# Kernel tuning notes

Hardware: AMD Instinct MI355X
Metric: run time of the kernel (lower is better)

Reference implementation:

```python
import jax, jax.numpy as jnp
import numpy as np

N_ATOMS = 100000   # real atoms (row 0 is padding => arrays have +1)
N_BONDS = 200000   # directed bonds (row 0 is padding)
MAX_NB = 6         # max incoming bonds per atom
ATOM_FDIM = 133
BOND_FDIM = 147
HIDDEN = 300
DEPTH = 3
NUM_MOLS = 2048


def setup_inputs() -> dict:
    key = jax.random.key(0)
    ks = jax.random.split(key, 10)
    f_atoms = jax.random.normal(ks[0], (N_ATOMS + 1, ATOM_FDIM), jnp.float32)
    f_bonds = jax.random.normal(ks[1], (N_BONDS + 1, BOND_FDIM), jnp.float32)
    # zero padding row, as in chemprop's BatchMolGraph
    f_atoms = f_atoms.at[0].set(0.0)
    f_bonds = f_bonds.at[0].set(0.0)
    W_i = jax.random.normal(ks[2], (BOND_FDIM, HIDDEN), jnp.float32) * 0.05
    W_h = jax.random.normal(ks[3], (HIDDEN, HIDDEN), jnp.float32) * 0.05
    W_o = jax.random.normal(ks[4], (ATOM_FDIM + HIDDEN, HIDDEN), jnp.float32) * 0.05
    b_o = jax.random.normal(ks[5], (HIDDEN,), jnp.float32) * 0.05
    a2b = jax.random.randint(ks[6], (N_ATOMS + 1, MAX_NB), 0, N_BONDS + 1, jnp.int32)
    b2a = jax.random.randint(ks[7], (N_BONDS + 1,), 0, N_ATOMS + 1, jnp.int32)
    b2revb = jax.random.randint(ks[8], (N_BONDS + 1,), 0, N_BONDS + 1, jnp.int32)
    # padding rows point at padding
    a2b = a2b.at[0].set(0)
    b2a = b2a.at[0].set(0)
    b2revb = b2revb.at[0].set(0)
    mol_ids = jax.random.randint(ks[9], (N_ATOMS,), 0, NUM_MOLS, jnp.int32)
    return {"f_atoms": f_atoms, "f_bonds": f_bonds, "W_i": W_i, "W_h": W_h,
            "W_o": W_o, "b_o": b_o, "a2b": a2b, "b2a": b2a,
            "b2revb": b2revb, "mol_ids": mol_ids}


def reference(f_atoms, f_bonds, W_i, W_h, W_o, b_o, a2b, b2a, b2revb, mol_ids):
    act = jax.nn.relu
    # input bond messages (W_i has no bias: args.bias=False)
    b_input = f_bonds @ W_i                      # [B+1, H]
    b_message = act(b_input)
    for _ in range(DEPTH - 1):
        # gather incoming bond messages per atom and sum over neighbors
        nei_a_message = b_message[a2b]           # [A+1, MAX_NB, H]
        a_message = nei_a_message.sum(axis=1)    # [A+1, H]
        # directed message update: m_uv = sum_in(v) - m_vu
        b_message = a_message[b2a] - b_message[b2revb]
        b_message = b_message @ W_h
        b_message = act(b_input + b_message)     # dropout p=0 omitted
    # atom readout
    nei_a_message = b_message[a2b]
    a_message = nei_a_message.sum(axis=1)        # [A+1, H]
    a_input = jnp.concatenate([f_atoms, a_message], axis=1)
    atom_hiddens = act(a_input @ W_o + b_o)      # [A+1, H]
    # mean-pool per molecule (a_scope readout), excluding padding row 0
    h = atom_hiddens[1:]                         # [A, H]
    sums = jax.ops.segment_sum(h, mol_ids, num_segments=NUM_MOLS)
    counts = jax.ops.segment_sum(jnp.ones((h.shape[0],), h.dtype), mol_ids,
                                 num_segments=NUM_MOLS)
    mol_vecs = sums / jnp.maximum(counts, 1.0)[:, None]  # [NUM_MOLS, H]
    return mol_vecs
```

## Files before the change

### kernel.cpp

```cpp
#include <hip/hip_runtime.h>

constexpr int N_ATOMS = 100000;
constexpr int NATOMS1 = 100001;
constexpr int NBONDS1 = 200001;
constexpr int MAXNB   = 6;
constexpr int AF      = 133;
constexpr int BF      = 147;
constexpr int H       = 300;
constexpr int NMOL    = 2048;
constexpr int KP      = 448;
constexpr int NP      = 320;
constexpr int QCOL_B  = 148;
constexpr int QCOL_A  = 136;
constexpr int QH      = 75;

typedef unsigned short u16;
typedef unsigned int   u32;
typedef __attribute__((ext_vector_type(8))) short bh8;
typedef __attribute__((ext_vector_type(4))) float f32x4;

__device__ inline float b2f(u16 h) {
    union { u32 u; float f; } x; x.u = ((u32)h) << 16; return x.f;
}
__device__ inline u16 f2b(float f) {
    union { float f; u32 u; } x; x.f = f;
    return (u16)((x.u + 0x7FFFu + ((x.u >> 16) & 1u)) >> 16);
}

template<bool HAS_BIAS>
__global__ __launch_bounds__(256, 2)
void mfma_gemm_k(const u16* __restrict__ A, const u16* __restrict__ Wt,
                 const float* __restrict__ bias, u16* __restrict__ out, int M)
{
    __shared__ __align__(16) unsigned char smem[48 * 1024];
    const int tid  = threadIdx.x;
    const int lane = tid & 63;
    const int w    = tid >> 6;
    const int row0 = blockIdx.x * 64;

    f32x4 acc[4][5];
    #pragma unroll
    for (int i = 0; i < 4; ++i)
        #pragma unroll
        for (int j = 0; j < 5; ++j)
            acc[i][j] = (f32x4)0.f;

    for (int kt = 0; kt < KP / 64; ++kt) {
        const int k0 = kt * 64;
        #pragma unroll
        for (int i = 0; i < 2; ++i) {
            int cid = tid + 256 * i;
            int r   = cid & 63;
            int kk  = cid >> 6;
            int ks  = kk >> 2, sub = kk & 3;
            uint4 v = {0u, 0u, 0u, 0u};
            int row = row0 + r;
            if (row < M) v = *(const uint4*)(A + (size_t)row * KP + k0 + kk * 8);
            *(uint4*)(smem + (((r >> 4) * 2 + ks) * 1024) + sub * 256 + (r & 15) * 16) = v;
        }
        #pragma unroll
        for (int i = 0; i < 10; ++i) {
            int cid = tid + 256 * i;
            int kk  = cid / 320;
            int col = cid - kk * 320;
            int ks  = kk >> 2, sub = kk & 3;
            uint4 v = *(const uint4*)(Wt + (size_t)col * KP + k0 + kk * 8);
            *(uint4*)(smem + 8192 + (((col >> 4) * 2 + ks) * 1024) + sub * 256 + (col & 15) * 16) = v;
        }
        __syncthreads();
        #pragma unroll
        for (int ks = 0; ks < 2; ++ks) {
            bh8 af[4], bf_[5];
            #pragma unroll
            for (int fm = 0; fm < 4; ++fm)
                af[fm] = *(const bh8*)(smem + (fm * 2 + ks) * 1024 + lane * 16);
            #pragma unroll
            for (int cf = 0; cf < 5; ++cf)
                bf_[cf] = *(const bh8*)(smem + 8192 + ((w * 5 + cf) * 2 + ks) * 1024 + lane * 16);
            #pragma unroll
            for (int fm = 0; fm < 4; ++fm)
                #pragma unroll
                for (int cf = 0; cf < 5; ++cf)
                    acc[fm][cf] = __builtin_amdgcn_mfma_f32_16x16x32_bf16(
                        af[fm], bf_[cf], acc[fm][cf], 0, 0, 0);
        }
        __syncthreads();
    }

    const int r4  = (lane >> 4) * 4;
    const int c15 = lane & 15;
    #pragma unroll
    for (int cf = 0; cf < 5; ++cf) {
        int col = w * 80 + cf * 16 + c15;
        if (col >= H) continue;
        float bv = HAS_BIAS ? bias[col] : 0.f;
        #pragma unroll
        for (int fm = 0; fm < 4; ++fm) {
            #pragma unroll
            for (int i = 0; i < 4; ++i) {
                int row = row0 + fm * 16 + r4 + i;
                if (row < M)
                    out[(size_t)row * H + col] = f2b(fmaxf(acc[fm][cf][i] + bv, 0.f));
            }
        }
    }
}

__global__ __launch_bounds__(256)
void prep_w_k(const float* __restrict__ Wi, const float* __restrict__ Wh,
              const float* __restrict__ Wo, u16* __restrict__ Wtih, u16* __restrict__ Wto)
{
    int c = blockIdx.x;
    for (int k = threadIdx.x; k < KP; k += 256) {
        u16 v1 = 0, v2 = 0;
        if (c < H) {
            if (k < BF)              v1 = f2b(Wi[k * H + c]);
            else if (k >= QCOL_B)    v1 = f2b(Wh[(k - QCOL_B) * H + c]);
            if (k < AF)              v2 = f2b(Wo[k * H + c]);
            else if (k >= QCOL_A && k < QCOL_A + H)
                                     v2 = f2b(Wo[(AF + k - QCOL_A) * H + c]);
        }
        Wtih[c * KP + k] = v1;
        Wto[c * KP + k]  = v2;
    }
}

__global__ __launch_bounds__(256)
void prep_bonds_k(const float* __restrict__ fb, u16* __restrict__ AB)
{
    int idx = blockIdx.x * 256 + threadIdx.x;
    if (idx >= NBONDS1 * (KP / 4)) return;
    int b = idx / (KP / 4), g = idx - b * (KP / 4);
    int c0 = g * 4;
    u16 o[4];
    #pragma unroll
    for (int j = 0; j < 4; ++j) {
        int c = c0 + j;
        o[j] = (c < BF) ? f2b(fb[(size_t)b * BF + c]) : (u16)0;
    }
    uint2 p;
    p.x = (u32)o[0] | ((u32)o[1] << 16);
    p.y = (u32)o[2] | ((u32)o[3] << 16);
    *(uint2*)(AB + (size_t)b * KP + c0) = p;
}

__global__ __launch_bounds__(256)
void prep_atoms_k(const float* __restrict__ fa, u16* __restrict__ AA)
{
    int idx = blockIdx.x * 256 + threadIdx.x;
    if (idx >= NATOMS1 * 37) return;
    int a = idx / 37, g = idx - a * 37;
    int c0 = (g < 34) ? g * 4 : 436 + (g - 34) * 4;
    u16 o[4];
    #pragma unroll
    for (int j = 0; j < 4; ++j) {
        int c = c0 + j;
        o[j] = (c < AF) ? f2b(fa[(size_t)a * AF + c]) : (u16)0;
    }
    uint2 p;
    p.x = (u32)o[0] | ((u32)o[1] << 16);
    p.y = (u32)o[2] | ((u32)o[3] << 16);
    *(uint2*)(AA + (size_t)a * KP + c0) = p;
}

__global__ __launch_bounds__(256)
void atom_sum_k(const u16* __restrict__ P, const int* __restrict__ a2b,
                u16* __restrict__ AA)
{
    int idx = blockIdx.x * 256 + threadIdx.x;
    if (idx >= NATOMS1 * QH) return;
    int a = idx / QH, q = idx - a * QH;
    const int* nb = a2b + a * MAXNB;
    float s0 = 0.f, s1 = 0.f, s2 = 0.f, s3 = 0.f;
    #pragma unroll
    for (int j = 0; j < MAXNB; ++j) {
        int b = nb[j];
        uint2 v = *(const uint2*)(P + (size_t)b * H + q * 4);
        s0 += b2f((u16)(v.x & 0xFFFF)); s1 += b2f((u16)(v.x >> 16));
        s2 += b2f((u16)(v.y & 0xFFFF)); s3 += b2f((u16)(v.y >> 16));
    }
    uint2 o;
    o.x = (u32)f2b(s0) | ((u32)f2b(s1) << 16);
    o.y = (u32)f2b(s2) | ((u32)f2b(s3) << 16);
    *(uint2*)(AA + (size_t)a * KP + QCOL_A + q * 4) = o;
}

__global__ __launch_bounds__(256)
void bond_update_k(const u16* __restrict__ AA, const u16* __restrict__ P,
                   const int* __restrict__ b2a, const int* __restrict__ b2revb,
                   u16* __restrict__ AB)
{
    int idx = blockIdx.x * 256 + threadIdx.x;
    if (idx >= NBONDS1 * QH) return;
    int b = idx / QH, q = idx - b * QH;
    int a  = b2a[b];
    int rb = b2revb[b];
    uint2 x = *(const uint2*)(AA + (size_t)a * KP + QCOL_A + q * 4);
    uint2 y = *(const uint2*)(P + (size_t)rb * H + q * 4);
    float v0 = b2f((u16)(x.x & 0xFFFF)) - b2f((u16)(y.x & 0xFFFF));
    float v1 = b2f((u16)(x.x >> 16))    - b2f((u16)(y.x >> 16));
    float v2 = b2f((u16)(x.y & 0xFFFF)) - b2f((u16)(y.y & 0xFFFF));
    float v3 = b2f((u16)(x.y >> 16))    - b2f((u16)(y.y >> 16));
    uint2 o;
    o.x = (u32)f2b(v0) | ((u32)f2b(v1) << 16);
    o.y = (u32)f2b(v2) | ((u32)f2b(v3) << 16);
    *(uint2*)(AB + (size_t)b * KP + QCOL_B + q * 4) = o;
}

__global__ __launch_bounds__(256)
void hist_k(const int* __restrict__ mol_ids, int* __restrict__ cnt)
{
    int i = blockIdx.x * 256 + threadIdx.x;
    if (i < N_ATOMS) atomicAdd(&cnt[mol_ids[i]], 1);
}

__global__ __launch_bounds__(256)
void scan_k(const int* __restrict__ cnt, int* __restrict__ offs)
{
    __shared__ int lds[256];
    const int t = threadIdx.x;
    int v[8];
    int s = 0;
    #pragma unroll
    for (int j = 0; j < 8; ++j) { v[j] = cnt[t * 8 + j]; s += v[j]; }
    lds[t] = s;
    __syncthreads();
    int run = s;
    #pragma unroll
    for (int d = 1; d < 256; d <<= 1) {
        int add = (t >= d) ? lds[t - d] : 0;
        __syncthreads();
        lds[t] += add;
        __syncthreads();
    }
    int excl = lds[t] - run;
    #pragma unroll
    for (int j = 0; j < 8; ++j) { offs[t * 8 + j] = excl; excl += v[j]; }
}

__global__ __launch_bounds__(256)
void fill_k(const int* __restrict__ mol_ids, const int* __restrict__ offs,
            int* __restrict__ fill, int* __restrict__ bucket)
{
    int i = blockIdx.x * 256 + threadIdx.x;
    if (i >= N_ATOMS) return;
    int m = mol_ids[i];
    int pos = offs[m] + atomicAdd(&fill[m], 1);
    bucket[pos] = i;
}

__global__ __launch_bounds__(320)
void mol_sum_k(const u16* __restrict__ ah, const int* __restrict__ offs,
               const int* __restrict__ cnt, const int* __restrict__ bucket,
               float* __restrict__ out)
{
    const int m = blockIdx.x;
    const int c = threadIdx.x;
    if (c >= H) return;
    const int start = offs[m];
    const int n     = cnt[m];
    float s = 0.f;
    for (int j = 0; j < n; ++j) {
        int a = bucket[start + j];
        s += b2f(ah[(size_t)(a + 1) * H + c]);
    }
    out[(size_t)m * H + c] = s / fmaxf((float)n, 1.0f);
}

extern "C" void kernel_launch(void* const* d_in, const int* in_sizes, int n_in,
                              void* d_out, int out_size, void* d_ws, size_t ws_size,
                              hipStream_t stream)
{
    const float* f_atoms = (const float*)d_in[0];
    const float* f_bonds = (const float*)d_in[1];
    const float* W_i     = (const float*)d_in[2];
    const float* W_h     = (const float*)d_in[3];
    const float* W_o     = (const float*)d_in[4];
    const float* b_o     = (const float*)d_in[5];
    const int*   a2b     = (const int*)d_in[6];
    const int*   b2a     = (const int*)d_in[7];
    const int*   b2revb  = (const int*)d_in[8];
    const int*   mol_ids = (const int*)d_in[9];
    float* out = (float*)d_out;

    char* ws = (char*)d_ws;
    size_t off = 0;
    auto alloc = [&](size_t bytes) -> void* {
        void* p = ws + off;
        off += (bytes + 255) & ~(size_t)255;
        return p;
    };
    u16* AB    = (u16*)alloc(sizeof(u16) * (size_t)NBONDS1 * KP);
    u16* AA    = (u16*)alloc(sizeof(u16) * (size_t)NATOMS1 * KP);
    u16* P     = (u16*)alloc(sizeof(u16) * (size_t)NBONDS1 * H);
    u16* Wtih  = (u16*)alloc(sizeof(u16) * (size_t)NP * KP);
    u16* Wto   = (u16*)alloc(sizeof(u16) * (size_t)NP * KP);
    int* cnt    = (int*)alloc(sizeof(int) * NMOL);
    int* offs   = (int*)alloc(sizeof(int) * NMOL);
    int* fill   = (int*)alloc(sizeof(int) * NMOL);
    int* bucket = (int*)alloc(sizeof(int) * N_ATOMS);
    const size_t needed = off;

    if (ws_size < needed) {
        hipMemsetAsync(d_out, 0, sizeof(float) * (size_t)NMOL * H, stream);
        return;
    }

    hipMemsetAsync(cnt, 0, sizeof(int) * NMOL, stream);
    hipMemsetAsync(fill, 0, sizeof(int) * NMOL, stream);

    const dim3 blk(256);
    const int gB  = (NBONDS1 + 63) / 64;
    const int gA  = (NATOMS1 + 63) / 64;
    const int gAS = (NATOMS1 * QH + 255) / 256;
    const int gBU = (NBONDS1 * QH + 255) / 256;

    prep_w_k<<<NP, blk, 0, stream>>>(W_i, W_h, W_o, Wtih, Wto);
    prep_bonds_k<<<(NBONDS1 * (KP / 4) + 255) / 256, blk, 0, stream>>>(f_bonds, AB);
    prep_atoms_k<<<(NATOMS1 * 37 + 255) / 256, blk, 0, stream>>>(f_atoms, AA);

    mfma_gemm_k<false><<<gB, blk, 0, stream>>>(AB, Wtih, nullptr, P, NBONDS1);

    for (int d = 0; d < 2; ++d) {
        atom_sum_k<<<gAS, blk, 0, stream>>>(P, a2b, AA);
        bond_update_k<<<gBU, blk, 0, stream>>>(AA, P, b2a, b2revb, AB);
        mfma_gemm_k<false><<<gB, blk, 0, stream>>>(AB, Wtih, nullptr, P, NBONDS1);
    }
    atom_sum_k<<<gAS, blk, 0, stream>>>(P, a2b, AA);

    mfma_gemm_k<true><<<gA, blk, 0, stream>>>(AA, Wto, b_o, P, NATOMS1);

    hist_k<<<(N_ATOMS + 255) / 256, blk, 0, stream>>>(mol_ids, cnt);
    scan_k<<<1, blk, 0, stream>>>(cnt, offs);
    fill_k<<<(N_ATOMS + 255) / 256, blk, 0, stream>>>(mol_ids, offs, fill, bucket);
    mol_sum_k<<<NMOL, dim3(320), 0, stream>>>(P, offs, cnt, bucket, out);
}
```

Measured before the change: 1.566 ms.

## Use direct global-to-LDS loads in MFMA GEMM with 5-wave blocks

Rewrites the bf16 MFMA GEMM to load A and weight tiles straight from global memory into LDS with global_load_lds, so the data no longer passes through registers. The K-step shrinks from 64 to 32, LDS drops from 48KB to 24KB, and blocks grow to 5 waves of 320 threads, each wave owning 64 output columns. The goal is higher occupancy and less load/store instruction overhead. In exchange there is no double buffering and twice as many barriers. The A row-bounds check is removed by padding the workspace to a multiple of 64 rows, and those padding rows are never initialized.

After: 1.425 ms. 1.1x faster.

```diff
diff --git a/kernel.cpp b/kernel.cpp
--- a/kernel.cpp
+++ b/kernel.cpp
@@ -13,6 +13,8 @@
 constexpr int QCOL_B  = 148;
 constexpr int QCOL_A  = 136;
 constexpr int QH      = 75;
+constexpr int NBP     = ((NBONDS1 + 63) / 64) * 64;
+constexpr int NAP     = ((NATOMS1 + 63) / 64) * 64;
 
 typedef unsigned short u16;
 typedef unsigned int   u32;
@@ -27,71 +29,76 @@
     return (u16)((x.u + 0x7FFFu + ((x.u >> 16) & 1u)) >> 16);
 }
 
+__device__ __forceinline__ void gld_lds16(const u16* g, unsigned char* l)
+{
+    __builtin_amdgcn_global_load_lds(
+        (const __attribute__((address_space(1))) unsigned int*)g,
+        (__attribute__((address_space(3))) unsigned int*)l,
+        16, 0, 0);
+}
+
 template<bool HAS_BIAS>
-__global__ __launch_bounds__(256, 2)
+__global__ __launch_bounds__(320, 4)
 void mfma_gemm_k(const u16* __restrict__ A, const u16* __restrict__ Wt,
                  const float* __restrict__ bias, u16* __restrict__ out, int M)
 {
-    __shared__ __align__(16) unsigned char smem[48 * 1024];
+    __shared__ __align__(16) unsigned char smem[24 * 1024];
     const int tid  = threadIdx.x;
     const int lane = tid & 63;
     const int w    = tid >> 6;
     const int row0 = blockIdx.x * 64;
 
-    f32x4 acc[4][5];
+    const u16* src[5];
+    unsigned char* dst[5];
+    #pragma unroll
+    for (int j = 0; j < 5; ++j) {
+        int r = w * 5 + j;
+        if (r < 4) {
+            src[j] = A + (size_t)(row0 + r * 16 + (lane & 15)) * KP + (lane >> 4) * 8;
+            dst[j] = smem + r * 1024 + lane * 16;
+        } else if (r < 24) {
+            int cb = r - 4;
+            src[j] = Wt + (size_t)(cb * 16 + (lane & 15)) * KP + (lane >> 4) * 8;
+            dst[j] = smem + 4096 + cb * 1024 + lane * 16;
+        } else {
+            src[j] = nullptr; dst[j] = nullptr;
+        }
+    }
+    const int njobs = (w == 4) ? 4 : 5;
+
+    f32x4 acc[4][4];
     #pragma unroll
     for (int i = 0; i < 4; ++i)
         #pragma unroll
+        for (int j = 0; j < 4; ++j)
+            acc[i][j] = (f32x4)0.f;
+
+    for (int kt = 0; kt < KP / 32; ++kt) {
+        #pragma unroll
         for (int j = 0; j < 5; ++j)
-            acc[i][j] = (f32x4)0.f;
-
-    for (int kt = 0; kt < KP / 64; ++kt) {
-        const int k0 = kt * 64;
-        #pragma unroll
-        for (int i = 0; i < 2; ++i) {
-            int cid = tid + 256 * i;
-            int r   = cid & 63;
-            int kk  = cid >> 6;
-            int ks  = kk >> 2, sub = kk & 3;
-            uint4 v = {0u, 0u, 0u, 0u};
-            int row = row0 + r;
-            if (row < M) v = *(const uint4*)(A + (size_t)row * KP + k0 + kk * 8);
-            *(uint4*)(smem + (((r >> 4) * 2 + ks) * 1024) + sub * 256 + (r & 15) * 16) = v;
-        }
-        #pragma unroll
-        for (int i = 0; i < 10; ++i) {
-            int cid = tid + 256 * i;
-            int kk  = cid / 320;
-            int col = cid - kk * 320;
-            int ks  = kk >> 2, sub = kk & 3;
-            uint4 v = *(const uint4*)(Wt + (size_t)col * KP + k0 + kk * 8);
-            *(uint4*)(smem + 8192 + (((col >> 4) * 2 + ks) * 1024) + sub * 256 + (col & 15) * 16) = v;
-        }
+            if (j < njobs) gld_lds16(src[j] + kt * 32, dst[j]);
         __syncthreads();
-        #pragma unroll
-        for (int ks = 0; ks < 2; ++ks) {
-            bh8 af[4], bf_[5];
+        bh8 af[4], bfr[4];
+        #pragma unroll
+        for (int fm = 0; fm < 4; ++fm)
+            af[fm] = *(const bh8*)(smem + fm * 1024 + lane * 16);
+        #pragma unroll
+        for (int cf = 0; cf < 4; ++cf)
+            bfr[cf] = *(const bh8*)(smem + 4096 + (w * 4 + cf) * 1024 + lane * 16);
+        #pragma unroll
+        for (int fm = 0; fm < 4; ++fm)
             #pragma unroll
-            for (int fm = 0; fm < 4; ++fm)
-                af[fm] = *(const bh8*)(smem + (fm * 2 + ks) * 1024 + lane * 16);
-            #pragma unroll
-            for (int cf = 0; cf < 5; ++cf)
-                bf_[cf] = *(const bh8*)(smem + 8192 + ((w * 5 + cf) * 2 + ks) * 1024 + lane * 16);
-            #pragma unroll
-            for (int fm = 0; fm < 4; ++fm)
-                #pragma unroll
-                for (int cf = 0; cf < 5; ++cf)
-                    acc[fm][cf] = __builtin_amdgcn_mfma_f32_16x16x32_bf16(
-                        af[fm], bf_[cf], acc[fm][cf], 0, 0, 0);
-        }
+            for (int cf = 0; cf < 4; ++cf)
+                acc[fm][cf] = __builtin_amdgcn_mfma_f32_16x16x32_bf16(
+                    af[fm], bfr[cf], acc[fm][cf], 0, 0, 0);
         __syncthreads();
     }
 
     const int r4  = (lane >> 4) * 4;
     const int c15 = lane & 15;
     #pragma unroll
-    for (int cf = 0; cf < 5; ++cf) {
-        int col = w * 80 + cf * 16 + c15;
+    for (int cf = 0; cf < 4; ++cf) {
+        int col = w * 64 + cf * 16 + c15;
         if (col >= H) continue;
         float bv = HAS_BIAS ? bias[col] : 0.f;
         #pragma unroll
@@ -290,8 +297,8 @@
         off += (bytes + 255) & ~(size_t)255;
         return p;
     };
-    u16* AB    = (u16*)alloc(sizeof(u16) * (size_t)NBONDS1 * KP);
-    u16* AA    = (u16*)alloc(sizeof(u16) * (size_t)NATOMS1 * KP);
+    u16* AB    = (u16*)alloc(sizeof(u16) * (size_t)NBP * KP);
+    u16* AA    = (u16*)alloc(sizeof(u16) * (size_t)NAP * KP);
     u16* P     = (u16*)alloc(sizeof(u16) * (size_t)NBONDS1 * H);
     u16* Wtih  = (u16*)alloc(sizeof(u16) * (size_t)NP * KP);
     u16* Wto   = (u16*)alloc(sizeof(u16) * (size_t)NP * KP);
@@ -310,8 +317,9 @@
     hipMemsetAsync(fill, 0, sizeof(int) * NMOL, stream);
 
     const dim3 blk(256);
-    const int gB  = (NBONDS1 + 63) / 64;
-    const int gA  = (NATOMS1 + 63) / 64;
+    const dim3 gblk(320);
+    const int gB  = NBP / 64;
+    const int gA  = NAP / 64;
     const int gAS = (NATOMS1 * QH + 255) / 256;
     const int gBU = (NBONDS1 * QH + 255) / 256;
 
@@ -319,19 +327,19 @@
     prep_bonds_k<<<(NBONDS1 * (KP / 4) + 255) / 256, blk, 0, stream>>>(f_bonds, AB);
     prep_atoms_k<<<(NATOMS1 * 37 + 255) / 256, blk, 0, stream>>>(f_atoms, AA);
 
-    mfma_gemm_k<false><<<gB, blk, 0, stream>>>(AB, Wtih, nullptr, P, NBONDS1);
+    mfma_gemm_k<false><<<gB, gblk, 0, stream>>>(AB, Wtih, nullptr, P, NBONDS1);
 
     for (int d = 0; d < 2; ++d) {
         atom_sum_k<<<gAS, blk, 0, stream>>>(P, a2b, AA);
         bond_update_k<<<gBU, blk, 0, stream>>>(AA, P, b2a, b2revb, AB);
-        mfma_gemm_k<false><<<gB, blk, 0, stream>>>(AB, Wtih, nullptr, P, NBONDS1);
+        mfma_gemm_k<false><<<gB, gblk, 0, stream>>>(AB, Wtih, nullptr, P, NBONDS1);
     }
     atom_sum_k<<<gAS, blk, 0, stream>>>(P, a2b, AA);
 
-    mfma_gemm_k<true><<<gA, blk, 0, stream>>>(AA, Wto, b_o, P, NATOMS1);
+    mfma_gemm_k<true><<<gA, gblk, 0, stream>>>(AA, Wto, b_o, P, NATOMS1);
 
     hist_k<<<(N_ATOMS + 255) / 256, blk, 0, stream>>>(mol_ids, cnt);
     scan_k<<<1, blk, 0, stream>>>(cnt, offs);
     fill_k<<<(N_ATOMS + 255) / 256, blk, 0, stream>>>(mol_ids, offs, fill, bucket);
-    mol_sum_k<<<NMOL, dim3(320), 0, stream>>>(P, offs, cnt, bucket, out);
-}
+    mol_sum_k<<<NMOL, gblk, 0, stream>>>(P, offs, cnt, bucket, out);
+}
```
